# Performance work log

Measured on AMD Instinct MI355X. Metric: run time of the kernel, lower is better.

## Reference

```python
import jax, jax.numpy as jnp
import numpy as np


def _ln(x, g, b, eps=1e-5):
    m = x.mean(-1, keepdims=True)
    v = ((x - m) ** 2).mean(-1, keepdims=True)
    return (x - m) * jax.lax.rsqrt(v + eps) * g + b


def _forward(x, norm1_g, norm1_b, in_proj_w, conv_w, x_proj_w, dt_projs_w,
             dt_projs_b, A_logs, Ds, out_norm_g, out_norm_b, out_proj_w,
             norm2_g, norm2_b, fc1_w, fc1_b, fc2_w, fc2_b):
    B, C, H, W = x.shape
    z = jnp.transpose(x, (0, 2, 3, 1))  # (B,H,W,C)

    # ---- SS2D branch (forward_type='v3noz': no z gate) ----
    u = _ln(z, norm1_g, norm1_b)
    u = u @ in_proj_w.T                       # (B,H,W,Din)
    Din = u.shape[-1]
    uc = jnp.transpose(u, (0, 3, 1, 2))       # (B,Din,H,W)
    uc = jax.lax.conv_general_dilated(
        uc, conv_w, (1, 1), 'SAME', feature_group_count=Din,
        dimension_numbers=('NCHW', 'OIHW', 'NCHW'))
    uc = jax.nn.silu(uc)

    L = H * W
    K = x_proj_w.shape[0]                     # 4 scan directions
    R = dt_projs_w.shape[-1]                  # dt_rank
    N = (x_proj_w.shape[1] - R) // 2          # d_state

    # cross-scan: row-major, col-major, and their reversals
    xf = uc.reshape(B, Din, L)
    xt = jnp.transpose(uc, (0, 1, 3, 2)).reshape(B, Din, L)
    xs = jnp.stack([xf, xt, xf[..., ::-1], xt[..., ::-1]], axis=1)  # (B,K,Din,L)

    dbl = jnp.einsum('bkdl,kcd->bkcl', xs, x_proj_w)
    dts, Bs, Cs = jnp.split(dbl, [R, R + N], axis=2)  # (B,K,R,L),(B,K,N,L),(B,K,N,L)
    dt = jax.nn.softplus(jnp.einsum('bkrl,kdr->bkdl', dts, dt_projs_w)
                         + dt_projs_b[None, :, :, None])  # (B,K,Din,L)
    A = -jnp.exp(A_logs).reshape(K, Din, N)

    # selective scan: h_t = exp(dt*A)*h_{t-1} + dt*B_t*u_t; via associative scan
    a = jnp.exp(dt[:, :, :, None, :] * A[None, :, :, :, None])          # (B,K,Din,N,L)
    bb = dt[:, :, :, None, :] * Bs[:, :, None, :, :] * xs[:, :, :, None, :]

    def comb(e1, e2):
        a1, b1 = e1
        a2, b2 = e2
        return a2 * a1, a2 * b1 + b2

    _, h = jax.lax.associative_scan(comb, (a, bb), axis=-1)
    y = jnp.einsum('bkdnl,bknl->bkdl', h, Cs) + Ds.reshape(K, Din)[None, :, :, None] * xs

    # cross-merge: undo reversals / transpose, then sum
    yr = y[:, 0] + y[:, 2][..., ::-1]
    yt = jnp.transpose((y[:, 1] + y[:, 3][..., ::-1]).reshape(B, Din, W, H),
                       (0, 1, 3, 2)).reshape(B, Din, L)
    ym = jnp.transpose((yr + yt).reshape(B, Din, H, W), (0, 2, 3, 1))  # (B,H,W,Din)

    ym = _ln(ym, out_norm_g, out_norm_b)
    z = z + ym @ out_proj_w.T

    # ---- MLP branch ----
    m = _ln(z, norm2_g, norm2_b)
    m = jax.nn.gelu(m @ fc1_w.T + fc1_b, approximate=False) @ fc2_w.T + fc2_b
    z = z + m

    # outer wrapper residual
    return x + jnp.transpose(z, (0, 3, 1, 2))


def setup_inputs() -> dict:
    key = jax.random.key(0)
    ks = jax.random.split(key, 10)
    dims, Din, R, N, K, dmlp = 96, 192, 6, 1, 4, 384
    B, H, W = 4, 64, 64
    f32 = jnp.float32
    return {
        'x': jax.random.normal(ks[0], (B, dims, H, W), f32),
        'norm1_g': jnp.ones((dims,), f32),
        'norm1_b': jnp.zeros((dims,), f32),
        'in_proj_w': jax.random.normal(ks[1], (Din, dims), f32) * 0.02,
        'conv_w': jax.random.normal(ks[2], (Din, 1, 3, 3), f32) * 0.1,
        'x_proj_w': jax.random.normal(ks[3], (K, R + 2 * N, Din), f32) * 0.02,
        'dt_projs_w': jax.random.normal(ks[4], (K, Din, R), f32) * 0.1,
        'dt_projs_b': jax.random.uniform(ks[5], (K, Din), f32) * 0.1,
        'A_logs': jnp.zeros((K * Din, N), f32),  # v0 init: A=arange(1,N+1) -> log=0 for N=1
        'Ds': jnp.ones((K * Din,), f32),
        'out_norm_g': jnp.ones((Din,), f32),
        'out_norm_b': jnp.zeros((Din,), f32),
        'out_proj_w': jax.random.normal(ks[6], (dims, Din), f32) * 0.02,
        'norm2_g': jnp.ones((dims,), f32),
        'norm2_b': jnp.zeros((dims,), f32),
        'fc1_w': jax.random.normal(ks[7], (dmlp, dims), f32) * 0.02,
        'fc1_b': jnp.zeros((dmlp,), f32),
        'fc2_w': jax.random.normal(ks[8], (dims, dmlp), f32) * 0.02,
        'fc2_b': jnp.zeros((dims,), f32),
    }


def reference(x, norm1_g, norm1_b, in_proj_w, conv_w, x_proj_w, dt_projs_w,
              dt_projs_b, A_logs, Ds, out_norm_g, out_norm_b, out_proj_w,
              norm2_g, norm2_b, fc1_w, fc1_b, fc2_w, fc2_b):
    return _forward(x, norm1_g, norm1_b, in_proj_w, conv_w, x_proj_w,
                    dt_projs_w, dt_projs_b, A_logs, Ds, out_norm_g, out_norm_b,
                    out_proj_w, norm2_g, norm2_b, fc1_w, fc1_b, fc2_w, fc2_b)
```

## Files before the change

### kernel.cpp

```cpp
#include <hip/hip_runtime.h>
#include <math.h>

namespace {

constexpr int Bn = 4, Cn = 96, Hn = 64, Wn = 64, Ln = 4096, Din = 192;
constexpr int Kn = 4, Rn = 6, Dmlp = 384;
constexpr int NCH = 128, CLEN = 32;

typedef short short8 __attribute__((ext_vector_type(8)));
typedef float f32x4 __attribute__((ext_vector_type(4)));

__device__ __forceinline__ float softplusf_(float x) {
  return fmaxf(x, 0.f) + __logf(1.f + __expf(-fabsf(x)));
}
__device__ __forceinline__ float siluf_(float x) {
  return x / (1.f + __expf(-x));
}
__device__ __forceinline__ float geluf_(float x) {
  return 0.5f * x * (1.f + erff(x * 0.7071067811865476f));
}
__device__ __forceinline__ unsigned short f2bf(float f) {
  unsigned u = __float_as_uint(f);
  unsigned r = 0x7fffu + ((u >> 16) & 1u);
  return (unsigned short)((u + r) >> 16);
}
__device__ __forceinline__ float bf2f(unsigned short v) {
  return __uint_as_float(((unsigned)v) << 16);
}

__global__ __launch_bounds__(256) void k1_ln_inproj(
    const float* __restrict__ x, const float* __restrict__ gam,
    const float* __restrict__ bet, const float* __restrict__ win,
    const float* __restrict__ w1, const float* __restrict__ w2,
    const float* __restrict__ wout, const float* __restrict__ wxp,
    unsigned short* __restrict__ ucpb, unsigned short* __restrict__ w1b,
    unsigned short* __restrict__ w2b, unsigned short* __restrict__ woutb,
    unsigned short* __restrict__ wxpb) {
  const int tid = threadIdx.x;
  if (blockIdx.x >= 512) {
    int t = (blockIdx.x - 512) * 256 + tid;
    if (t < 36864) w1b[t] = f2bf(w1[t]);
    else if (t < 73728) w2b[t - 36864] = f2bf(w2[t - 36864]);
    else if (t < 92160) woutb[t - 73728] = f2bf(wout[t - 73728]);
    else wxpb[t - 92160] = f2bf(wxp[t - 92160]);
    return;
  }

  __shared__ float sx[32 * 97];
  __shared__ __align__(16) unsigned short smb[32 * 104];
  __shared__ __align__(16) unsigned short swin[192 * 96];
  const int p0 = blockIdx.x * 32;
  const int b = p0 >> 12, pl0 = p0 & (Ln - 1);

  for (int e = tid; e < 4608; e += 256) {
    float4 w4 = reinterpret_cast<const float4*>(win)[e];
    uint2 pk;
    pk.x = (unsigned)f2bf(w4.x) | ((unsigned)f2bf(w4.y) << 16);
    pk.y = (unsigned)f2bf(w4.z) | ((unsigned)f2bf(w4.w) << 16);
    *reinterpret_cast<uint2*>(&swin[e * 4]) = pk;
  }

  for (int f = tid; f < 32 * 96; f += 256) {
    int c = f >> 5, pp = f & 31;
    sx[pp * 97 + c] = x[((size_t)b * Cn + c) * Ln + pl0 + pp];
  }
  __syncthreads();
  {
    const int pp = tid >> 3, t8 = tid & 7;
    float s = 0.f;
    for (int c = t8 * 12; c < t8 * 12 + 12; ++c) s += sx[pp * 97 + c];
    s += __shfl_xor(s, 1, 8); s += __shfl_xor(s, 2, 8); s += __shfl_xor(s, 4, 8);
    float m = s * (1.f / 96.f);
    float v = 0.f;
    for (int c = t8 * 12; c < t8 * 12 + 12; ++c) {
      float t = sx[pp * 97 + c] - m; v += t * t;
    }
    v += __shfl_xor(v, 1, 8); v += __shfl_xor(v, 2, 8); v += __shfl_xor(v, 4, 8);
    float rs = rsqrtf(v * (1.f / 96.f) + 1e-5f);
    for (int c = t8 * 12; c < t8 * 12 + 12; ++c)
      sx[pp * 97 + c] = (sx[pp * 97 + c] - m) * rs * gam[c] + bet[c];
  }
  __syncthreads();
  for (int f = tid; f < 32 * 96; f += 256) {
    int pp = f / 96, c = f % 96;
    smb[pp * 104 + c] = f2bf(sx[pp * 97 + c]);
  }
  __syncthreads();

  const int wv = tid >> 6, lane = tid & 63;
  const int l15 = lane & 15, lhi = lane >> 4;
  const int mt = wv & 1, nbase = (wv >> 1) * 6;
  for (int t = 0; t < 6; ++t) {
    const int n0 = (nbase + t) * 16;
    f32x4 acc = {0.f, 0.f, 0.f, 0.f};
#pragma unroll
    for (int kk = 0; kk < 3; ++kk) {
      short8 av = *reinterpret_cast<const short8*>(
          &smb[(16 * mt + l15) * 104 + kk * 32 + lhi * 8]);
      short8 bv = *reinterpret_cast<const short8*>(
          &swin[(n0 + l15) * 96 + kk * 32 + lhi * 8]);
      acc = __builtin_amdgcn_mfma_f32_16x16x32_bf16(av, bv, acc, 0, 0, 0);
    }
    const int j = n0 + l15;
    uint2 pk;
    pk.x = (unsigned)f2bf(acc[0]) | ((unsigned)f2bf(acc[1]) << 16);
    pk.y = (unsigned)f2bf(acc[2]) | ((unsigned)f2bf(acc[3]) << 16);
    *reinterpret_cast<uint2*>(
        &ucpb[((size_t)b * Din + j) * Ln + pl0 + 16 * mt + lhi * 4]) = pk;
  }
}

__global__ __launch_bounds__(512) void k2a_conv(
    const unsigned short* __restrict__ ucpb, const float* __restrict__ cw,
    unsigned short* __restrict__ utb) {
  __shared__ float su[64 * 97];
  const int tid = threadIdx.x;
  const int bid = blockIdx.x;
  const int half = bid & 1, bh = bid >> 1;
  const int b = bh >> 6, h = bh & 63;
  const int w = tid & 63, wg = tid >> 6;
  const int d0 = half * 96;

  for (int dd = 0; dd < 12; ++dd) {
    int dl = wg * 12 + dd;
    int d = d0 + dl;
    const unsigned short* base = &ucpb[((size_t)b * Din + d) * Ln];
    float r0 = (h > 0) ? bf2f(base[(h - 1) * 64 + w]) : 0.f;
    float r1 = bf2f(base[h * 64 + w]);
    float r2 = (h < 63) ? bf2f(base[(h + 1) * 64 + w]) : 0.f;
    const float* wt = &cw[d * 9];
    float rl, rr, acc;
    rl = __shfl(r0, (w + 63) & 63); if (w == 0) rl = 0.f;
    rr = __shfl(r0, (w + 1) & 63);  if (w == 63) rr = 0.f;
    acc = rl * wt[0] + r0 * wt[1] + rr * wt[2];
    rl = __shfl(r1, (w + 63) & 63); if (w == 0) rl = 0.f;
    rr = __shfl(r1, (w + 1) & 63);  if (w == 63) rr = 0.f;
    acc += rl * wt[3] + r1 * wt[4] + rr * wt[5];
    rl = __shfl(r2, (w + 63) & 63); if (w == 0) rl = 0.f;
    rr = __shfl(r2, (w + 1) & 63);  if (w == 63) rr = 0.f;
    acc += rl * wt[6] + r2 * wt[7] + rr * wt[8];
    su[w * 97 + dl] = siluf_(acc);
  }
  __syncthreads();

  for (int f = tid; f < 768; f += 512) {
    int pp = f / 12, c8 = (f % 12) * 8;
    short8 v;
#pragma unroll
    for (int j = 0; j < 8; ++j) v[j] = (short)f2bf(su[pp * 97 + c8 + j]);
    *reinterpret_cast<short8*>(
        &utb[((size_t)b * Ln + h * 64 + pp) * Din + d0 + c8]) = v;
  }
}

__global__ __launch_bounds__(256) void k2b_xproj(
    const unsigned short* __restrict__ utb,
    const unsigned short* __restrict__ wxpb, float* __restrict__ dblp) {
  __shared__ __align__(16) unsigned short sa[32 * 200];
  const int tid = threadIdx.x;
  const int p0 = blockIdx.x * 32;

  for (int f = tid; f < 768; f += 256) {
    int pp = f / 24, c8 = f % 24;
    *reinterpret_cast<short8*>(&sa[pp * 200 + c8 * 8]) =
        *reinterpret_cast<const short8*>(&utb[(size_t)(p0 + pp) * 192 + c8 * 8]);
  }
  __syncthreads();

  const int wv = tid >> 6, lane = tid & 63;
  const int l15 = lane & 15, lhi = lane >> 4;
  const int mt = wv & 1, n0 = (wv >> 1) * 16;
  f32x4 acc = {0.f, 0.f, 0.f, 0.f};
#pragma unroll
  for (int kk = 0; kk < 6; ++kk) {
    short8 av = *reinterpret_cast<const short8*>(
        &sa[(16 * mt + l15) * 200 + kk * 32 + lhi * 8]);
    short8 bv = *reinterpret_cast<const short8*>(
        &wxpb[(size_t)(n0 + l15) * 192 + kk * 32 + lhi * 8]);
    acc = __builtin_amdgcn_mfma_f32_16x16x32_bf16(av, bv, acc, 0, 0, 0);
  }
  const int q = n0 + l15;
#pragma unroll
  for (int r = 0; r < 4; ++r) {
    int px = 16 * mt + lhi * 4 + r;
    dblp[(size_t)(p0 + px) * 32 + q] = acc[r];
  }
}

__device__ __forceinline__ int scan_pixel(int k, int l) {
  if (k == 0) return l;
  if (k == 1) return ((l & 63) << 6) | (l >> 6);
  if (k == 2) return Ln - 1 - l;
  int m2 = Ln - 1 - l;
  return ((m2 & 63) << 6) | (m2 >> 6);
}

__global__ __launch_bounds__(192) void k4_scan1(
    const unsigned short* __restrict__ utb, const float* __restrict__ dblp,
    const float* __restrict__ wdtg, const float* __restrict__ bdtg,
    const float* __restrict__ alog, float* __restrict__ apb,
    float* __restrict__ heb) {
  __shared__ __align__(16) float sdb[CLEN * 8];
  const int bid = blockIdx.x;
  const int ch = bid & (NCH - 1);
  const int bk = bid / NCH;
  const int b = bk >> 2, k = bk & 3;
  const int d = threadIdx.x;
  const int l0 = ch * CLEN;

  for (int f = d; f < CLEN * 8; f += 192) {
    int i = f >> 3, c8 = f & 7;
    int p = scan_pixel(k, l0 + i);
    sdb[f] = dblp[((size_t)b * Ln + p) * 32 + k * 8 + c8];
  }

  float wdt[6];
#pragma unroll
  for (int r = 0; r < 6; ++r) wdt[r] = wdtg[(k * Din + d) * 6 + r];
  const float bdt = bdtg[k * Din + d];
  const float Av = -__expf(alog[k * Din + d]);
  const unsigned short* ub = &utb[(size_t)b * Ln * Din];
  __syncthreads();

  float h = 0.f, ap = 1.f;
  for (int i0 = 0; i0 < CLEN; i0 += 8) {
    float U[8];
#pragma unroll
    for (int j = 0; j < 8; ++j) {
      int p = scan_pixel(k, l0 + i0 + j);
      U[j] = bf2f(ub[(size_t)p * Din + d]);
    }
#pragma unroll
    for (int j = 0; j < 8; ++j) {
      float4 qa = *reinterpret_cast<const float4*>(&sdb[(i0 + j) * 8]);
      float4 qb = *reinterpret_cast<const float4*>(&sdb[(i0 + j) * 8 + 4]);
      float xdt = bdt;
      xdt = fmaf(qa.x, wdt[0], xdt); xdt = fmaf(qa.y, wdt[1], xdt);
      xdt = fmaf(qa.z, wdt[2], xdt); xdt = fmaf(qa.w, wdt[3], xdt);
      xdt = fmaf(qb.x, wdt[4], xdt); xdt = fmaf(qb.y, wdt[5], xdt);
      float dt = softplusf_(xdt);
      float a = __expf(dt * Av);
      float bbv = dt * qb.z * U[j];
      h = fmaf(a, h, bbv);
      ap *= a;
    }
  }
  size_t o = ((size_t)bk * NCH + ch) * Din + d;
  apb[o] = ap;
  heb[o] = h;
}

__global__ __launch_bounds__(192) void k6_scan2(
    const unsigned short* __restrict__ utb, const float* __restrict__ dblp,
    const float* __restrict__ wdtg, const float* __restrict__ bdtg,
    const float* __restrict__ alog, const float* __restrict__ dsg,
    const float* __restrict__ apb, const float* __restrict__ heb,
    unsigned short* __restrict__ yd) {
  __shared__ __align__(16) float sdb[CLEN * 8];
  __shared__ __align__(16) unsigned short ys[CLEN * 192];
  const int bid = blockIdx.x;
  const int ch = bid & (NCH - 1);
  const int bk = bid / NCH;
  const int b = bk >> 2, k = bk & 3;
  const int d = threadIdx.x;
  const int l0 = ch * CLEN;

  for (int f = d; f < CLEN * 8; f += 192) {
    int i = f >> 3, c8 = f & 7;
    int p = scan_pixel(k, l0 + i);
    sdb[f] = dblp[((size_t)b * Ln + p) * 32 + k * 8 + c8];
  }

  float wdt[6];
#pragma unroll
  for (int r = 0; r < 6; ++r) wdt[r] = wdtg[(k * Din + d) * 6 + r];
  const float bdt = bdtg[k * Din + d];
  const float Av = -__expf(alog[k * Din + d]);
  const float Dv = dsg[k * Din + d];
  const unsigned short* ub = &utb[(size_t)b * Ln * Din];
  unsigned short* yk = &yd[(size_t)bk * Ln * Din];

  float h = 0.f;
  {
    const float* ap_ = &apb[(size_t)bk * NCH * Din + d];
    const float* hp_ = &heb[(size_t)bk * NCH * Din + d];
    int j0 = 0;
    for (; j0 + 8 <= ch; j0 += 8) {
      float A[8], H[8];
#pragma unroll
      for (int jj = 0; jj < 8; ++jj) {
        A[jj] = ap_[(size_t)(j0 + jj) * Din];
        H[jj] = hp_[(size_t)(j0 + jj) * Din];
      }
#pragma unroll
      for (int jj = 0; jj < 8; ++jj) h = fmaf(A[jj], h, H[jj]);
    }
    for (; j0 < ch; ++j0)
      h = fmaf(ap_[(size_t)j0 * Din], h, hp_[(size_t)j0 * Din]);
  }
  __syncthreads();

  for (int i0 = 0; i0 < CLEN; i0 += 8) {
    float U[8];
#pragma unroll
    for (int j = 0; j < 8; ++j) {
      int p = scan_pixel(k, l0 + i0 + j);
      U[j] = bf2f(ub[(size_t)p * Din + d]);
    }
#pragma unroll
    for (int j = 0; j < 8; ++j) {
      float4 qa = *reinterpret_cast<const float4*>(&sdb[(i0 + j) * 8]);
      float4 qb = *reinterpret_cast<const float4*>(&sdb[(i0 + j) * 8 + 4]);
      float xdt = bdt;
      xdt = fmaf(qa.x, wdt[0], xdt); xdt = fmaf(qa.y, wdt[1], xdt);
      xdt = fmaf(qa.z, wdt[2], xdt); xdt = fmaf(qa.w, wdt[3], xdt);
      xdt = fmaf(qb.x, wdt[4], xdt); xdt = fmaf(qb.y, wdt[5], xdt);
      float dt = softplusf_(xdt);
      float a = __expf(dt * Av);
      float bbv = dt * qb.z * U[j];
      h = fmaf(a, h, bbv);
      ys[(i0 + j) * 192 + d] = f2bf(h * qb.w + Dv * U[j]);
    }
  }
  __syncthreads();
  for (int e = d; e < CLEN * 24; e += 192) {
    *reinterpret_cast<short8*>(&yk[(size_t)l0 * 192 + e * 8]) =
        *reinterpret_cast<const short8*>(&ys[e * 8]);
  }
}

__global__ __launch_bounds__(256) void k78_tail(
    const unsigned short* __restrict__ yd, const float* __restrict__ gam,
    const float* __restrict__ bet, const unsigned short* __restrict__ woutb,
    const float* __restrict__ g2, const float* __restrict__ b2,
    const unsigned short* __restrict__ w1b, const float* __restrict__ b1f,
    const unsigned short* __restrict__ w2b, const float* __restrict__ b2f,
    const float* __restrict__ x, float* __restrict__ out) {
  __shared__ __align__(16) char smem[50304];
  float* SY = (float*)smem;
  unsigned short* SB7 = (unsigned short*)(smem + 24704);
  unsigned short* SH = (unsigned short*)(smem + 37504);
  float* SZ = (float*)smem;
  unsigned short* SM = (unsigned short*)(smem + 12416);
  float* SMLP = (float*)(smem + 24704);

  const int tid = threadIdx.x;
  const int p0 = blockIdx.x * 32;
  const int b = p0 >> 12, pl0 = p0 & (Ln - 1);
  const int wv = tid >> 6, lane = tid & 63;
  const int l15 = lane & 15, lhi = lane >> 4;

  {
    const unsigned short* y0b = &yd[(size_t)(b * 4 + 0) * Ln * Din];
    const unsigned short* y1b = &yd[(size_t)(b * 4 + 1) * Ln * Din];
    const unsigned short* y2b = &yd[(size_t)(b * 4 + 2) * Ln * Din];
    const unsigned short* y3b = &yd[(size_t)(b * 4 + 3) * Ln * Din];
    for (int f = tid; f < 32 * 24; f += 256) {
      int pp = f / 24, c8 = (f % 24) * 8;
      int p = pl0 + pp;
      int l1 = ((p & 63) << 6) | (p >> 6);
      short8 v0 = *reinterpret_cast<const short8*>(&y0b[(size_t)p * 192 + c8]);
      short8 v2 = *reinterpret_cast<const short8*>(
          &y2b[(size_t)(Ln - 1 - p) * 192 + c8]);
      short8 v1 = *reinterpret_cast<const short8*>(&y1b[(size_t)l1 * 192 + c8]);
      short8 v3 = *reinterpret_cast<const short8*>(
          &y3b[(size_t)(Ln - 1 - l1) * 192 + c8]);
#pragma unroll
      for (int j = 0; j < 8; ++j)
        SY[pp * 193 + c8 + j] =
            bf2f((unsigned short)v0[j]) + bf2f((unsigned short)v2[j]) +
            bf2f((unsigned short)v1[j]) + bf2f((unsigned short)v3[j]);
    }
  }
  __syncthreads();

  {
    const int pp = tid >> 3, t8 = tid & 7;
    float s = 0.f;
    for (int d2 = t8 * 24; d2 < t8 * 24 + 24; ++d2) s += SY[pp * 193 + d2];
    s += __shfl_xor(s, 1, 8); s += __shfl_xor(s, 2, 8); s += __shfl_xor(s, 4, 8);
    float m = s * (1.f / 192.f);
    float v = 0.f;
    for (int d2 = t8 * 24; d2 < t8 * 24 + 24; ++d2) {
      float t = SY[pp * 193 + d2] - m; v += t * t;
    }
    v += __shfl_xor(v, 1, 8); v += __shfl_xor(v, 2, 8); v += __shfl_xor(v, 4, 8);
    float rs = rsqrtf(v * (1.f / 192.f) + 1e-5f);
    for (int d2 = t8 * 24; d2 < t8 * 24 + 24; ++d2)
      SB7[pp * 200 + d2] = f2bf((SY[pp * 193 + d2] - m) * rs * gam[d2] + bet[d2]);
  }
  __syncthreads();

  for (int q = 0; q < 3; ++q) {
    const int tt = wv + q * 4;
    const int mt = tt & 1, c0 = (tt >> 1) * 16;
    f32x4 acc = {0.f, 0.f, 0.f, 0.f};
#pragma unroll
    for (int kk = 0; kk < 6; ++kk) {
      short8 av = *reinterpret_cast<const short8*>(
          &SB7[(16 * mt + l15) * 200 + kk * 32 + lhi * 8]);
      short8 bv = *reinterpret_cast<const short8*>(
          &woutb[(size_t)(c0 + l15) * 192 + kk * 32 + lhi * 8]);
      acc = __builtin_amdgcn_mfma_f32_16x16x32_bf16(av, bv, acc, 0, 0, 0);
    }
    const int c = c0 + l15;
#pragma unroll
    for (int r = 0; r < 4; ++r) {
      int px = 16 * mt + lhi * 4 + r;
      SZ[px * 97 + c] = acc[r];
    }
  }
  __syncthreads();

  float xr[12];
#pragma unroll
  for (int it = 0; it < 12; ++it) {
    int f = tid + it * 256;
    int c = f >> 5, pp = f & 31;
    xr[it] = x[((size_t)b * Cn + c) * Ln + pl0 + pp];
    SZ[pp * 97 + c] += xr[it];
  }
  __syncthreads();

  {
    const int pp = tid >> 3, t8 = tid & 7;
    float s = 0.f;
    for (int c = t8 * 12; c < t8 * 12 + 12; ++c) s += SZ[pp * 97 + c];
    s += __shfl_xor(s, 1, 8); s += __shfl_xor(s, 2, 8); s += __shfl_xor(s, 4, 8);
    float m = s * (1.f / 96.f);
    float v = 0.f;
    for (int c = t8 * 12; c < t8 * 12 + 12; ++c) {
      float t = SZ[pp * 97 + c] - m; v += t * t;
    }
    v += __shfl_xor(v, 1, 8); v += __shfl_xor(v, 2, 8); v += __shfl_xor(v, 4, 8);
    float rs = rsqrtf(v * (1.f / 96.f) + 1e-5f);
    for (int c = t8 * 12; c < t8 * 12 + 12; ++c)
      SM[pp * 104 + c] = f2bf((SZ[pp * 97 + c] - m) * rs * g2[c] + b2[c]);
  }
  __syncthreads();

  f32x4 acc2[3];
#pragma unroll
  for (int q = 0; q < 3; ++q) acc2[q] = (f32x4){0.f, 0.f, 0.f, 0.f};

  for (int hlf = 0; hlf < 2; ++hlf) {
    {
      const int mt = wv & 1;
      const int ngrp = (wv >> 1) * 6;
      for (int t = 0; t < 6; ++t) {
        const int n0 = (ngrp + t) * 16;
        f32x4 acc = {0.f, 0.f, 0.f, 0.f};
#pragma unroll
        for (int kk = 0; kk < 3; ++kk) {
          short8 av = *reinterpret_cast<const short8*>(
              &SM[(16 * mt + l15) * 104 + kk * 32 + lhi * 8]);
          short8 bv = *reinterpret_cast<const short8*>(
              &w1b[(size_t)(hlf * 192 + n0 + l15) * 96 + kk * 32 + lhi * 8]);
          acc = __builtin_amdgcn_mfma_f32_16x16x32_bf16(av, bv, acc, 0, 0, 0);
        }
        const int jl = n0 + l15;
        const float bj = b1f[hlf * 192 + jl];
#pragma unroll
        for (int r = 0; r < 4; ++r) {
          int px = 16 * mt + lhi * 4 + r;
          SH[px * 200 + jl] = f2bf(geluf_(acc[r] + bj));
        }
      }
    }
    __syncthreads();
    for (int q = 0; q < 3; ++q) {
      const int tt = wv + q * 4;
      const int mt = tt & 1, c0 = (tt >> 1) * 16;
#pragma unroll
      for (int kk = 0; kk < 6; ++kk) {
        short8 av = *reinterpret_cast<const short8*>(
            &SH[(16 * mt + l15) * 200 + kk * 32 + lhi * 8]);
        short8 bv = *reinterpret_cast<const short8*>(
            &w2b[(size_t)(c0 + l15) * 384 + hlf * 192 + kk * 32 + lhi * 8]);
        acc2[q] = __builtin_amdgcn_mfma_f32_16x16x32_bf16(av, bv, acc2[q], 0, 0, 0);
      }
    }
    __syncthreads();
  }

  for (int q = 0; q < 3; ++q) {
    const int tt = wv + q * 4;
    const int mt = tt & 1, c0 = (tt >> 1) * 16;
    const int c = c0 + l15;
    const float bc = b2f[c];
#pragma unroll
    for (int r = 0; r < 4; ++r) {
      int px = 16 * mt + lhi * 4 + r;
      SMLP[px * 97 + c] = acc2[q][r] + bc;
    }
  }
  __syncthreads();

#pragma unroll
  for (int it = 0; it < 12; ++it) {
    int f = tid + it * 256;
    int c = f >> 5, pp = f & 31;
    out[((size_t)b * Cn + c) * Ln + pl0 + pp] =
        xr[it] + SZ[pp * 97 + c] + SMLP[pp * 97 + c];
  }
}

}

extern "C" void kernel_launch(void* const* d_in, const int* in_sizes, int n_in,
                              void* d_out, int out_size, void* d_ws,
                              size_t ws_size, hipStream_t stream) {
  const float* x        = (const float*)d_in[0];
  const float* norm1_g  = (const float*)d_in[1];
  const float* norm1_b  = (const float*)d_in[2];
  const float* in_proj  = (const float*)d_in[3];
  const float* conv_w   = (const float*)d_in[4];
  const float* x_proj   = (const float*)d_in[5];
  const float* dt_w     = (const float*)d_in[6];
  const float* dt_b     = (const float*)d_in[7];
  const float* A_logs   = (const float*)d_in[8];
  const float* Ds       = (const float*)d_in[9];
  const float* onorm_g  = (const float*)d_in[10];
  const float* onorm_b  = (const float*)d_in[11];
  const float* out_proj = (const float*)d_in[12];
  const float* norm2_g  = (const float*)d_in[13];
  const float* norm2_b  = (const float*)d_in[14];
  const float* fc1_w    = (const float*)d_in[15];
  const float* fc1_b    = (const float*)d_in[16];
  const float* fc2_w    = (const float*)d_in[17];
  const float* fc2_b    = (const float*)d_in[18];
  float* out = (float*)d_out;

  float* ws = (float*)d_ws;
  size_t o = 0;
  float* dblp = ws + o; o += (size_t)Bn * Ln * 32;
  float* apb  = ws + o; o += (size_t)Bn * Kn * NCH * Din;
  float* heb  = ws + o; o += (size_t)Bn * Kn * NCH * Din;
  unsigned short* ucpb = (unsigned short*)(ws + o); o += (size_t)Bn * Din * Ln / 2;
  unsigned short* utb  = (unsigned short*)(ws + o); o += (size_t)Bn * Ln * Din / 2;
  unsigned short* yd   = (unsigned short*)(ws + o); o += (size_t)Bn * Kn * Ln * Din / 2;
  unsigned short* w1b = (unsigned short*)(ws + o); o += 36864 / 2;
  unsigned short* w2b = (unsigned short*)(ws + o); o += 36864 / 2;
  unsigned short* woutb = (unsigned short*)(ws + o); o += 18432 / 2;
  unsigned short* wxpb = (unsigned short*)(ws + o); o += 6144 / 2;

  k1_ln_inproj<<<896, 256, 0, stream>>>(x, norm1_g, norm1_b, in_proj, fc1_w,
                                        fc2_w, out_proj, x_proj, ucpb, w1b,
                                        w2b, woutb, wxpb);
  k2a_conv<<<Bn * Hn * 2, 512, 0, stream>>>(ucpb, conv_w, utb);
  k2b_xproj<<<512, 256, 0, stream>>>(utb, wxpb, dblp);
  k4_scan1<<<Bn * Kn * NCH, 192, 0, stream>>>(utb, dblp, dt_w, dt_b, A_logs,
                                              apb, heb);
  k6_scan2<<<Bn * Kn * NCH, 192, 0, stream>>>(utb, dblp, dt_w, dt_b, A_logs,
                                              Ds, apb, heb, yd);
  k78_tail<<<512, 256, 0, stream>>>(yd, onorm_g, onorm_b, woutb, norm2_g,
                                    norm2_b, w1b, fc1_b, w2b, fc2_b, x, out);
}
```

Baseline: 106.6 us.

## Fuse x_proj GEMM into both scan kernels and stage inputs in LDS

Removes the separate x_proj kernel and its dblp buffer. Each scan block now loads its 32-pixel chunk of the conv output into shared memory with vector loads, computes its direction's 8 projection columns with MFMA, and reads U from LDS instead of doing strided scalar global loads. This drops one launch and the dblp write/read round trip. In exchange the projection GEMM is computed twice (once in each scan pass) and LDS use per block goes up, which may lower occupancy.

```diff
diff --git a/kernel.cpp b/kernel.cpp
--- a/kernel.cpp
+++ b/kernel.cpp
@@ -153,40 +153,6 @@
   }
 }
 
-__global__ __launch_bounds__(256) void k2b_xproj(
-    const unsigned short* __restrict__ utb,
-    const unsigned short* __restrict__ wxpb, float* __restrict__ dblp) {
-  __shared__ __align__(16) unsigned short sa[32 * 200];
-  const int tid = threadIdx.x;
-  const int p0 = blockIdx.x * 32;
-
-  for (int f = tid; f < 768; f += 256) {
-    int pp = f / 24, c8 = f % 24;
-    *reinterpret_cast<short8*>(&sa[pp * 200 + c8 * 8]) =
-        *reinterpret_cast<const short8*>(&utb[(size_t)(p0 + pp) * 192 + c8 * 8]);
-  }
-  __syncthreads();
-
-  const int wv = tid >> 6, lane = tid & 63;
-  const int l15 = lane & 15, lhi = lane >> 4;
-  const int mt = wv & 1, n0 = (wv >> 1) * 16;
-  f32x4 acc = {0.f, 0.f, 0.f, 0.f};
-#pragma unroll
-  for (int kk = 0; kk < 6; ++kk) {
-    short8 av = *reinterpret_cast<const short8*>(
-        &sa[(16 * mt + l15) * 200 + kk * 32 + lhi * 8]);
-    short8 bv = *reinterpret_cast<const short8*>(
-        &wxpb[(size_t)(n0 + l15) * 192 + kk * 32 + lhi * 8]);
-    acc = __builtin_amdgcn_mfma_f32_16x16x32_bf16(av, bv, acc, 0, 0, 0);
-  }
-  const int q = n0 + l15;
-#pragma unroll
-  for (int r = 0; r < 4; ++r) {
-    int px = 16 * mt + lhi * 4 + r;
-    dblp[(size_t)(p0 + px) * 32 + q] = acc[r];
-  }
-}
-
 __device__ __forceinline__ int scan_pixel(int k, int l) {
   if (k == 0) return l;
   if (k == 1) return ((l & 63) << 6) | (l >> 6);
@@ -195,11 +161,47 @@
   return ((m2 & 63) << 6) | (m2 >> 6);
 }
 
+__device__ __forceinline__ void scan_stage(
+    const unsigned short* __restrict__ ub,
+    const unsigned short* __restrict__ wxpb, int k, int l0, int d,
+    unsigned short* su, float* sdb) {
+  for (int e = d; e < 768; e += 192) {
+    int i = e / 24, c8 = (e % 24) * 8;
+    int p = scan_pixel(k, l0 + i);
+    *reinterpret_cast<short8*>(&su[i * 200 + c8]) =
+        *reinterpret_cast<const short8*>(&ub[(size_t)p * 192 + c8]);
+  }
+  __syncthreads();
+  const int wv3 = d >> 6, lane = d & 63;
+  const int l15 = lane & 15, lhi = lane >> 4;
+  if (wv3 < 2) {
+    const int mt = wv3;
+    const int n0 = (k >> 1) * 16;
+    f32x4 acc = {0.f, 0.f, 0.f, 0.f};
+#pragma unroll
+    for (int kk = 0; kk < 6; ++kk) {
+      short8 av = *reinterpret_cast<const short8*>(
+          &su[(16 * mt + l15) * 200 + kk * 32 + lhi * 8]);
+      short8 bv = *reinterpret_cast<const short8*>(
+          &wxpb[(size_t)(n0 + l15) * 192 + kk * 32 + lhi * 8]);
+      acc = __builtin_amdgcn_mfma_f32_16x16x32_bf16(av, bv, acc, 0, 0, 0);
+    }
+    if ((l15 >> 3) == (k & 1)) {
+      const int c8 = l15 & 7;
+#pragma unroll
+      for (int r = 0; r < 4; ++r)
+        sdb[(16 * mt + lhi * 4 + r) * 8 + c8] = acc[r];
+    }
+  }
+  __syncthreads();
+}
+
 __global__ __launch_bounds__(192) void k4_scan1(
-    const unsigned short* __restrict__ utb, const float* __restrict__ dblp,
-    const float* __restrict__ wdtg, const float* __restrict__ bdtg,
-    const float* __restrict__ alog, float* __restrict__ apb,
-    float* __restrict__ heb) {
+    const unsigned short* __restrict__ utb,
+    const unsigned short* __restrict__ wxpb, const float* __restrict__ wdtg,
+    const float* __restrict__ bdtg, const float* __restrict__ alog,
+    float* __restrict__ apb, float* __restrict__ heb) {
+  __shared__ __align__(16) unsigned short su[32 * 200];
   __shared__ __align__(16) float sdb[CLEN * 8];
   const int bid = blockIdx.x;
   const int ch = bid & (NCH - 1);
@@ -208,28 +210,19 @@
   const int d = threadIdx.x;
   const int l0 = ch * CLEN;
 
-  for (int f = d; f < CLEN * 8; f += 192) {
-    int i = f >> 3, c8 = f & 7;
-    int p = scan_pixel(k, l0 + i);
-    sdb[f] = dblp[((size_t)b * Ln + p) * 32 + k * 8 + c8];
-  }
-
   float wdt[6];
 #pragma unroll
   for (int r = 0; r < 6; ++r) wdt[r] = wdtg[(k * Din + d) * 6 + r];
   const float bdt = bdtg[k * Din + d];
   const float Av = -__expf(alog[k * Din + d]);
-  const unsigned short* ub = &utb[(size_t)b * Ln * Din];
-  __syncthreads();
+
+  scan_stage(&utb[(size_t)b * Ln * Din], wxpb, k, l0, d, su, sdb);
 
   float h = 0.f, ap = 1.f;
   for (int i0 = 0; i0 < CLEN; i0 += 8) {
     float U[8];
 #pragma unroll
-    for (int j = 0; j < 8; ++j) {
-      int p = scan_pixel(k, l0 + i0 + j);
-      U[j] = bf2f(ub[(size_t)p * Din + d]);
-    }
+    for (int j = 0; j < 8; ++j) U[j] = bf2f(su[(i0 + j) * 200 + d]);
 #pragma unroll
     for (int j = 0; j < 8; ++j) {
       float4 qa = *reinterpret_cast<const float4*>(&sdb[(i0 + j) * 8]);
@@ -251,11 +244,12 @@
 }
 
 __global__ __launch_bounds__(192) void k6_scan2(
-    const unsigned short* __restrict__ utb, const float* __restrict__ dblp,
-    const float* __restrict__ wdtg, const float* __restrict__ bdtg,
-    const float* __restrict__ alog, const float* __restrict__ dsg,
-    const float* __restrict__ apb, const float* __restrict__ heb,
-    unsigned short* __restrict__ yd) {
+    const unsigned short* __restrict__ utb,
+    const unsigned short* __restrict__ wxpb, const float* __restrict__ wdtg,
+    const float* __restrict__ bdtg, const float* __restrict__ alog,
+    const float* __restrict__ dsg, const float* __restrict__ apb,
+    const float* __restrict__ heb, unsigned short* __restrict__ yd) {
+  __shared__ __align__(16) unsigned short su[32 * 200];
   __shared__ __align__(16) float sdb[CLEN * 8];
   __shared__ __align__(16) unsigned short ys[CLEN * 192];
   const int bid = blockIdx.x;
@@ -265,19 +259,12 @@
   const int d = threadIdx.x;
   const int l0 = ch * CLEN;
 
-  for (int f = d; f < CLEN * 8; f += 192) {
-    int i = f >> 3, c8 = f & 7;
-    int p = scan_pixel(k, l0 + i);
-    sdb[f] = dblp[((size_t)b * Ln + p) * 32 + k * 8 + c8];
-  }
-
   float wdt[6];
 #pragma unroll
   for (int r = 0; r < 6; ++r) wdt[r] = wdtg[(k * Din + d) * 6 + r];
   const float bdt = bdtg[k * Din + d];
   const float Av = -__expf(alog[k * Din + d]);
   const float Dv = dsg[k * Din + d];
-  const unsigned short* ub = &utb[(size_t)b * Ln * Din];
   unsigned short* yk = &yd[(size_t)bk * Ln * Din];
 
   float h = 0.f;
@@ -298,15 +285,13 @@
     for (; j0 < ch; ++j0)
       h = fmaf(ap_[(size_t)j0 * Din], h, hp_[(size_t)j0 * Din]);
   }
-  __syncthreads();
+
+  scan_stage(&utb[(size_t)b * Ln * Din], wxpb, k, l0, d, su, sdb);
 
   for (int i0 = 0; i0 < CLEN; i0 += 8) {
     float U[8];
 #pragma unroll
-    for (int j = 0; j < 8; ++j) {
-      int p = scan_pixel(k, l0 + i0 + j);
-      U[j] = bf2f(ub[(size_t)p * Din + d]);
-    }
+    for (int j = 0; j < 8; ++j) U[j] = bf2f(su[(i0 + j) * 200 + d]);
 #pragma unroll
     for (int j = 0; j < 8; ++j) {
       float4 qa = *reinterpret_cast<const float4*>(&sdb[(i0 + j) * 8]);
@@ -533,7 +518,6 @@
 
   float* ws = (float*)d_ws;
   size_t o = 0;
-  float* dblp = ws + o; o += (size_t)Bn * Ln * 32;
   float* apb  = ws + o; o += (size_t)Bn * Kn * NCH * Din;
   float* heb  = ws + o; o += (size_t)Bn * Kn * NCH * Din;
   unsigned short* ucpb = (unsigned short*)(ws + o); o += (size_t)Bn * Din * Ln / 2;
@@ -548,10 +532,9 @@
                                         fc2_w, out_proj, x_proj, ucpb, w1b,
                                         w2b, woutb, wxpb);
   k2a_conv<<<Bn * Hn * 2, 512, 0, stream>>>(ucpb, conv_w, utb);
-  k2b_xproj<<<512, 256, 0, stream>>>(utb, wxpb, dblp);
-  k4_scan1<<<Bn * Kn * NCH, 192, 0, stream>>>(utb, dblp, dt_w, dt_b, A_logs,
+  k4_scan1<<<Bn * Kn * NCH, 192, 0, stream>>>(utb, wxpb, dt_w, dt_b, A_logs,
                                               apb, heb);
-  k6_scan2<<<Bn * Kn * NCH, 192, 0, stream>>>(utb, dblp, dt_w, dt_b, A_logs,
+  k6_scan2<<<Bn * Kn * NCH, 192, 0, stream>>>(utb, wxpb, dt_w, dt_b, A_logs,
                                               Ds, apb, heb, yd);
   k78_tail<<<512, 256, 0, stream>>>(yd, onorm_g, onorm_b, woutb, norm2_g,
                                     norm2_b, w1b, fc1_b, w2b, fc2_b, x, out);
```

Result: faster. 103.3 us (-3.1%).
